# Kernel optimization log

Measured on AMD Instinct MI355X. Metric: run time of the kernel, lower is better.

Reference implementation:

```python
import jax, jax.numpy as jnp
import numpy as np

N = 169343
EPS = 1e-5


def gcn_norm(edge_index, n):
    """GCN normalization with self-loops: returns per-edge norm and per-node self-loop norm."""
    dst = edge_index[1]
    deg = jnp.ones((n,), jnp.float32).at[dst].add(1.0)  # in-degree + self loop
    dinv = jax.lax.rsqrt(deg)
    edge_norm = dinv[edge_index[0]] * dinv[dst]          # [E]
    self_norm = 1.0 / deg                                 # deg^-1/2 * deg^-1/2
    return edge_norm, self_norm


def gcn_conv(x, W, b, edge_index, edge_norm, self_norm):
    h = x @ W                                             # [N, out]
    msg = h[edge_index[0]] * edge_norm[:, None]           # gather + scale, [E, out]
    agg = jax.ops.segment_sum(msg, edge_index[1], num_segments=N)
    return agg + h * self_norm[:, None] + b


def batch_norm(x, gamma, beta, mean, var):
    return (x - mean) * jax.lax.rsqrt(var + EPS) * gamma + beta


def setup_inputs() -> dict:
    key = jax.random.key(0)
    ks = jax.random.split(key, 12)
    E = 2400000
    d_in, d_h, d_out = 128, 256, 40
    inp = {
        "x": jax.random.normal(ks[0], (N, d_in), jnp.float32),
        "edge_index": jax.random.randint(ks[1], (2, E), 0, N, jnp.int64),
        "W1": jax.random.normal(ks[2], (d_in, d_h), jnp.float32) / np.sqrt(d_in),
        "b1": jnp.zeros((d_h,), jnp.float32),
        "g1": 1.0 + 0.1 * jax.random.normal(ks[3], (d_h,), jnp.float32),
        "beta1": 0.1 * jax.random.normal(ks[4], (d_h,), jnp.float32),
        "m1": 0.1 * jax.random.normal(ks[5], (d_h,), jnp.float32),
        "v1": jnp.ones((d_h,), jnp.float32),
        "W2": jax.random.normal(ks[6], (d_h, d_h), jnp.float32) / np.sqrt(d_h),
        "b2": jnp.zeros((d_h,), jnp.float32),
        "g2": 1.0 + 0.1 * jax.random.normal(ks[7], (d_h,), jnp.float32),
        "beta2": 0.1 * jax.random.normal(ks[8], (d_h,), jnp.float32),
        "m2": 0.1 * jax.random.normal(ks[9], (d_h,), jnp.float32),
        "v2": jnp.ones((d_h,), jnp.float32),
        "W3": jax.random.normal(ks[10], (d_h, d_out), jnp.float32) / np.sqrt(d_h),
        "b3": jnp.zeros((d_out,), jnp.float32),
    }
    return inp


def reference(x, edge_index, W1, b1, g1, beta1, m1, v1, W2, b2, g2, beta2, m2, v2, W3, b3):
    # eval mode: BN uses running stats, dropout is identity
    edge_norm, self_norm = gcn_norm(edge_index, N)
    h = gcn_conv(x, W1, b1, edge_index, edge_norm, self_norm)
    h = jax.nn.relu(batch_norm(h, g1, beta1, m1, v1))
    h = gcn_conv(h, W2, b2, edge_index, edge_norm, self_norm)
    h = jax.nn.relu(batch_norm(h, g2, beta2, m2, v2))
    node_embeddings = h
    out = gcn_conv(h, W3, b3, edge_index, edge_norm, self_norm)
    out = jax.nn.log_softmax(out, axis=-1)
    return out, node_embeddings
```

## Files before the change

kernel.cpp:

```cpp
#include <hip/hip_runtime.h>
#include <math.h>

#define EPSV 1e-5f
#define NBMAX 680

typedef __attribute__((ext_vector_type(8))) short bf16x8;
typedef __attribute__((ext_vector_type(4))) float floatx4;

__device__ __forceinline__ unsigned short f32_to_bf16(float f) {
    unsigned int u = __float_as_uint(f);
    unsigned int r = (u + 0x7fffu + ((u >> 16) & 1u)) >> 16;
    return (unsigned short)r;
}
__device__ __forceinline__ float bf16_lo(unsigned int u) { return __uint_as_float(u << 16); }
__device__ __forceinline__ float bf16_hi(unsigned int u) { return __uint_as_float(u & 0xffff0000u); }


__global__ __launch_bounds__(256) void zero_int_kernel(int* __restrict__ p, int n) {
    int i = blockIdx.x * 256 + threadIdx.x;
    if (i < n) p[i] = 0;
}

__global__ __launch_bounds__(256) void bucket_hist_kernel(const int* __restrict__ ei,
                                                          int* __restrict__ hist,
                                                          int* __restrict__ btot,
                                                          int E, int nb) {
    __shared__ int lh[NBMAX];
    int t = threadIdx.x;
    for (int i = t; i < nb; i += 256) lh[i] = 0;
    __syncthreads();
    int chunk = (E + 255) >> 8;
    int beg = blockIdx.x * chunk;
    int end = min(beg + chunk, E);
    for (int e = beg + t; e < end; e += 256) {
        int d = ei[E + e];
        atomicAdd(&lh[d >> 8], 1);
    }
    __syncthreads();
    for (int i = t; i < nb; i += 256) {
        int v = lh[i];
        hist[i * 256 + blockIdx.x] = v;
        if (v) atomicAdd(&btot[i], v);
    }
}

__global__ __launch_bounds__(256) void bucket_offsets_kernel(const int* __restrict__ btot,
                                                             int* __restrict__ hist,
                                                             int* __restrict__ bbase, int E) {
    __shared__ int red[256];
    __shared__ int sa[256], sb[256];
    int b = blockIdx.x, t = threadIdx.x;
    int s = 0;
    for (int i = t; i < b; i += 256) s += btot[i];
    red[t] = s;
    __syncthreads();
    for (int off = 128; off > 0; off >>= 1) {
        if (t < off) red[t] += red[t + off];
        __syncthreads();
    }
    int mybase = red[0];
    if (t == 0) {
        bbase[b] = mybase;
        if (b == gridDim.x - 1) bbase[gridDim.x] = E;
    }
    int orig = hist[b * 256 + t];
    sa[t] = orig;
    __syncthreads();
    int* sp = sa; int* dp = sb;
    for (int off = 1; off < 256; off <<= 1) {
        int x = sp[t] + (t >= off ? sp[t - off] : 0);
        dp[t] = x;
        __syncthreads();
        int* q = sp; sp = dp; dp = q;
    }
    hist[b * 256 + t] = mybase + sp[t] - orig;
}

__global__ __launch_bounds__(256) void bin_kernel(const int* __restrict__ ei,
                                                  const int* __restrict__ hist,
                                                  unsigned int* __restrict__ tmp,
                                                  int E, int nb) {
    __shared__ int cur[NBMAX];
    int t = threadIdx.x;
    for (int i = t; i < nb; i += 256) cur[i] = hist[i * 256 + blockIdx.x];
    __syncthreads();
    int chunk = (E + 255) >> 8;
    int beg = blockIdx.x * chunk;
    int end = min(beg + chunk, E);
    for (int e = beg + t; e < end; e += 256) {
        int s = ei[e];
        int d = ei[E + e];
        int pos = atomicAdd(&cur[d >> 8], 1);
        tmp[pos] = ((unsigned int)(d & 255) << 24) | (unsigned int)s;
    }
}

__global__ __launch_bounds__(256) void bucket_sort_kernel(const unsigned int* __restrict__ tmp,
                                                          const int* __restrict__ bbase,
                                                          int* __restrict__ rowptr,
                                                          int* __restrict__ csr,
                                                          float* __restrict__ dinv,
                                                          float* __restrict__ selfnorm,
                                                          int n, int E) {
    __shared__ int cnt[256];
    __shared__ int sa[256], sb[256];
    int b = blockIdx.x, t = threadIdx.x;
    int node0 = b << 8;
    int nn = min(256, n - node0);
    int ebeg = bbase[b], eend = bbase[b + 1];
    cnt[t] = 0;
    __syncthreads();
    for (int e = ebeg + t; e < eend; e += 256) {
        unsigned int v = tmp[e];
        atomicAdd(&cnt[v >> 24], 1);
    }
    __syncthreads();
    sa[t] = cnt[t];
    __syncthreads();
    int* sp = sa; int* dp = sb;
    for (int off = 1; off < 256; off <<= 1) {
        int x = sp[t] + (t >= off ? sp[t - off] : 0);
        dp[t] = x;
        __syncthreads();
        int* q = sp; sp = dp; dp = q;
    }
    int excl = sp[t] - cnt[t];
    if (t < nn) {
        rowptr[node0 + t] = ebeg + excl;
        float df = (float)(cnt[t] + 1);
        dinv[node0 + t] = rsqrtf(df);
        selfnorm[node0 + t] = 1.0f / df;
    }
    if (b == gridDim.x - 1 && t == 0) rowptr[n] = E;
    dp[t] = ebeg + excl;
    __syncthreads();
    for (int e = ebeg + t; e < eend; e += 256) {
        unsigned int v = tmp[e];
        int lpos = atomicAdd(&dp[v >> 24], 1);
        csr[lpos] = (int)(v & 0xFFFFFFu);
    }
}


__global__ __launch_bounds__(256) void cast_bf16_kernel(const float* __restrict__ in,
                                                        unsigned short* __restrict__ out, int n4) {
    int i = blockIdx.x * 256 + threadIdx.x;
    if (i < n4) {
        float4 f = ((const float4*)in)[i];
        ushort4 o;
        o.x = f32_to_bf16(f.x); o.y = f32_to_bf16(f.y);
        o.z = f32_to_bf16(f.z); o.w = f32_to_bf16(f.w);
        ((ushort4*)out)[i] = o;
    }
}

__global__ __launch_bounds__(256) void cast_transpose_kernel(const float* __restrict__ in,
                                                             unsigned short* __restrict__ out,
                                                             int K, int M) {
    int i = blockIdx.x * 256 + threadIdx.x;
    if (i < K * M) {
        int k = i / M, m2 = i - k * M;
        out[(size_t)m2 * K + k] = f32_to_bf16(in[i]);
    }
}


__device__ __forceinline__ void acc8(float* acc, uint4 u, float wt) {
    acc[0] += wt * bf16_lo(u.x); acc[1] += wt * bf16_hi(u.x);
    acc[2] += wt * bf16_lo(u.y); acc[3] += wt * bf16_hi(u.y);
    acc[4] += wt * bf16_lo(u.z); acc[5] += wt * bf16_hi(u.z);
    acc[6] += wt * bf16_lo(u.w); acc[7] += wt * bf16_hi(u.w);
}

template <int LPN>
__global__ __launch_bounds__(256) void agg_pre_kernel(const unsigned short* __restrict__ h,
                                                      const int* __restrict__ rowptr,
                                                      const int* __restrict__ csr,
                                                      const float* __restrict__ dinv,
                                                      const float* __restrict__ selfnorm,
                                                      unsigned short* __restrict__ z, int n) {
    const int W = LPN * 8;
    int gtid = blockIdx.x * 256 + threadIdx.x;
    int node = gtid / LPN;
    int sub = gtid % LPN;
    if (node >= n) return;
    int fb = sub * 8;
    const unsigned short* hb = h + fb;
    int beg = rowptr[node], end = rowptr[node + 1];

    float acc[8] = {0.f, 0.f, 0.f, 0.f, 0.f, 0.f, 0.f, 0.f};
    int e = beg;
    for (; e + 4 <= end; e += 4) {
        int s0 = csr[e], s1 = csr[e + 1], s2 = csr[e + 2], s3 = csr[e + 3];
        float w0 = dinv[s0], w1 = dinv[s1], w2 = dinv[s2], w3 = dinv[s3];
        uint4 u0 = *(const uint4*)(hb + (size_t)s0 * W);
        uint4 u1 = *(const uint4*)(hb + (size_t)s1 * W);
        uint4 u2 = *(const uint4*)(hb + (size_t)s2 * W);
        uint4 u3 = *(const uint4*)(hb + (size_t)s3 * W);
        acc8(acc, u0, w0); acc8(acc, u1, w1); acc8(acc, u2, w2); acc8(acc, u3, w3);
    }
    for (; e < end; ++e) {
        int s = csr[e];
        float w = dinv[s];
        uint4 u = *(const uint4*)(hb + (size_t)s * W);
        acc8(acc, u, w);
    }
    float di = dinv[node], sn = selfnorm[node];
    uint4 us = *(const uint4*)(hb + (size_t)node * W);
    float hs[8];
    hs[0] = bf16_lo(us.x); hs[1] = bf16_hi(us.x);
    hs[2] = bf16_lo(us.y); hs[3] = bf16_hi(us.y);
    hs[4] = bf16_lo(us.z); hs[5] = bf16_hi(us.z);
    hs[6] = bf16_lo(us.w); hs[7] = bf16_hi(us.w);
    float o[8];
#pragma unroll
    for (int j = 0; j < 8; ++j) o[j] = acc[j] * di + hs[j] * sn;
    uint4 ov;
    ov.x = ((unsigned int)f32_to_bf16(o[1]) << 16) | f32_to_bf16(o[0]);
    ov.y = ((unsigned int)f32_to_bf16(o[3]) << 16) | f32_to_bf16(o[2]);
    ov.z = ((unsigned int)f32_to_bf16(o[5]) << 16) | f32_to_bf16(o[4]);
    ov.w = ((unsigned int)f32_to_bf16(o[7]) << 16) | f32_to_bf16(o[6]);
    *(uint4*)(z + (size_t)node * W + fb) = ov;
}


__global__ __launch_bounds__(256) void gemm_bf16_kernel(
    const unsigned short* __restrict__ A, const unsigned short* __restrict__ Wt,
    unsigned short* __restrict__ Cb, int cstride, float* __restrict__ Cf,
    const float* __restrict__ bias, const float* __restrict__ g,
    const float* __restrict__ beta, const float* __restrict__ m,
    const float* __restrict__ v, int nrows, int K, int M) {
    __shared__ short As[64 * 40];
    __shared__ short Bs[64 * 40];
    int tid = threadIdx.x;
    int wave = tid >> 6, lane = tid & 63;
    int quad = lane >> 4, l16 = lane & 15;
    int wr = (wave >> 1) * 32, wc = (wave & 1) * 32;
    int row0 = blockIdx.x * 64, col0 = blockIdx.y * 64;

    int srow = tid >> 2, sseg = tid & 3;

    floatx4 acc[2][2];
#pragma unroll
    for (int i = 0; i < 2; ++i)
#pragma unroll
        for (int j = 0; j < 2; ++j)
#pragma unroll
            for (int r = 0; r < 4; ++r) acc[i][j][r] = 0.f;

    for (int k0 = 0; k0 < K; k0 += 32) {
        uint4 av = make_uint4(0, 0, 0, 0);
        int gr = row0 + srow;
        if (gr < nrows) av = *(const uint4*)(A + (size_t)gr * K + k0 + sseg * 8);
        uint4 bv = make_uint4(0, 0, 0, 0);
        int gc = col0 + srow;
        if (gc < M) bv = *(const uint4*)(Wt + (size_t)gc * K + k0 + sseg * 8);

        *(uint4*)(As + srow * 40 + sseg * 8) = av;
        *(uint4*)(Bs + srow * 40 + sseg * 8) = bv;
        __syncthreads();

        bf16x8 af[2], bfr[2];
#pragma unroll
        for (int i = 0; i < 2; ++i)
            af[i] = *(const bf16x8*)(As + (wr + i * 16 + l16) * 40 + quad * 8);
#pragma unroll
        for (int j = 0; j < 2; ++j)
            bfr[j] = *(const bf16x8*)(Bs + (wc + j * 16 + l16) * 40 + quad * 8);

#pragma unroll
        for (int i = 0; i < 2; ++i)
#pragma unroll
            for (int j = 0; j < 2; ++j)
                acc[i][j] = __builtin_amdgcn_mfma_f32_16x16x32_bf16(af[i], bfr[j], acc[i][j], 0, 0, 0);
        __syncthreads();
    }

    float sc[2], sh[2];
#pragma unroll
    for (int j = 0; j < 2; ++j) {
        int col = col0 + wc + j * 16 + l16;
        if (bias && col < M) {
            float s = g[col] * rsqrtf(v[col] + EPSV);
            sc[j] = s;
            sh[j] = (bias[col] - m[col]) * s + beta[col];
        } else {
            sc[j] = 1.f; sh[j] = 0.f;
        }
    }

#pragma unroll
    for (int i = 0; i < 2; ++i) {
#pragma unroll
        for (int r = 0; r < 4; ++r) {
            int row = row0 + wr + i * 16 + quad * 4 + r;
            if (row >= nrows) continue;
#pragma unroll
            for (int j = 0; j < 2; ++j) {
                int col = col0 + wc + j * 16 + l16;
                if (col < M) {
                    float val = acc[i][j][r];
                    if (bias) val = fmaxf(val * sc[j] + sh[j], 0.f);
                    if (Cb) Cb[(size_t)row * cstride + col] = f32_to_bf16(val);
                    if (Cf) Cf[(size_t)row * M + col] = val;
                }
            }
        }
    }
}


__global__ __launch_bounds__(256) void agg3_lsm_kernel(const unsigned short* __restrict__ h3,
                                                       const int* __restrict__ rowptr,
                                                       const int* __restrict__ csr,
                                                       const float* __restrict__ dinv,
                                                       const float* __restrict__ selfnorm,
                                                       const float* __restrict__ b3,
                                                       float* __restrict__ out, int n) {
    int node = (blockIdx.x * 256 + threadIdx.x) >> 6;
    int lane = threadIdx.x & 63;
    if (node >= n) return;
    int sub = lane & 15, grp = lane >> 4;
    int beg = rowptr[node], end = rowptr[node + 1];
    const unsigned short* hb = h3 + sub * 4;

    float acc[4] = {0.f, 0.f, 0.f, 0.f};
    int e = beg + grp;
    for (; e + 4 < end; e += 8) {
        int s0 = csr[e], s1 = csr[e + 4];
        float w0 = dinv[s0], w1 = dinv[s1];
        uint2 u0 = *(const uint2*)(hb + (size_t)s0 * 64);
        uint2 u1 = *(const uint2*)(hb + (size_t)s1 * 64);
        acc[0] += w0 * bf16_lo(u0.x); acc[1] += w0 * bf16_hi(u0.x);
        acc[2] += w0 * bf16_lo(u0.y); acc[3] += w0 * bf16_hi(u0.y);
        acc[0] += w1 * bf16_lo(u1.x); acc[1] += w1 * bf16_hi(u1.x);
        acc[2] += w1 * bf16_lo(u1.y); acc[3] += w1 * bf16_hi(u1.y);
    }
    for (; e < end; e += 4) {
        int s = csr[e];
        float w = dinv[s];
        uint2 u = *(const uint2*)(hb + (size_t)s * 64);
        acc[0] += w * bf16_lo(u.x); acc[1] += w * bf16_hi(u.x);
        acc[2] += w * bf16_lo(u.y); acc[3] += w * bf16_hi(u.y);
    }
#pragma unroll
    for (int j = 0; j < 4; ++j) {
        acc[j] += __shfl_xor(acc[j], 16, 64);
        acc[j] += __shfl_xor(acc[j], 32, 64);
    }
    float di = dinv[node], sn = selfnorm[node];
    uint2 us = *(const uint2*)(h3 + (size_t)node * 64 + sub * 4);
    float self4[4] = {bf16_lo(us.x), bf16_hi(us.x), bf16_lo(us.y), bf16_hi(us.y)};
    int f0 = sub * 4;
    float z[4];
#pragma unroll
    for (int j = 0; j < 4; ++j) {
        int f = f0 + j;
        int fc = f < 40 ? f : 0;
        float val = acc[j] * di + self4[j] * sn + b3[fc];
        z[j] = (f < 40) ? val : -INFINITY;
    }
    float mx = fmaxf(fmaxf(z[0], z[1]), fmaxf(z[2], z[3]));
#pragma unroll
    for (int off = 1; off < 16; off <<= 1) mx = fmaxf(mx, __shfl_xor(mx, off, 64));
    float se = expf(z[0] - mx) + expf(z[1] - mx) + expf(z[2] - mx) + expf(z[3] - mx);
#pragma unroll
    for (int off = 1; off < 16; off <<= 1) se += __shfl_xor(se, off, 64);
    float lse = logf(se);
    if (grp == 0 && sub < 10) {
        float4 o = make_float4(z[0] - mx - lse, z[1] - mx - lse, z[2] - mx - lse, z[3] - mx - lse);
        *(float4*)(out + (size_t)node * 40 + f0) = o;
    }
}


extern "C" void kernel_launch(void* const* d_in, const int* in_sizes, int n_in,
                              void* d_out, int out_size, void* d_ws, size_t ws_size,
                              hipStream_t stream) {
    const float* x  = (const float*)d_in[0];
    const int* ei   = (const int*)d_in[1];
    const float* W1 = (const float*)d_in[2];
    const float* b1 = (const float*)d_in[3];
    const float* g1 = (const float*)d_in[4];
    const float* be1 = (const float*)d_in[5];
    const float* m1 = (const float*)d_in[6];
    const float* v1 = (const float*)d_in[7];
    const float* W2 = (const float*)d_in[8];
    const float* b2 = (const float*)d_in[9];
    const float* g2 = (const float*)d_in[10];
    const float* be2 = (const float*)d_in[11];
    const float* m2 = (const float*)d_in[12];
    const float* v2 = (const float*)d_in[13];
    const float* W3 = (const float*)d_in[14];
    const float* b3 = (const float*)d_in[15];

    const int N = in_sizes[0] / 128;
    const int E = in_sizes[1] / 2;
    const int nb = (N + 255) >> 8;

    float* out_lsm = (float*)d_out;
    float* out_emb = (float*)d_out + (size_t)N * 40;

    char* ws = (char*)d_ws;
    size_t off = 0;
    auto carve = [&](size_t bytes) -> void* {
        void* p = ws + off;
        off = (off + bytes + 255) & ~(size_t)255;
        return p;
    };
    int* hist     = (int*)carve((size_t)nb * 256 * 4);
    int* btot     = (int*)carve((size_t)nb * 4);
    int* bbase    = (int*)carve((size_t)(nb + 1) * 4);
    int* rowptr   = (int*)carve((size_t)(N + 1) * 4);
    int* csr      = (int*)carve((size_t)E * 4);
    float* dinv     = (float*)carve((size_t)N * 4);
    float* selfnorm = (float*)carve((size_t)N * 4);
    unsigned short* W1t = (unsigned short*)carve((size_t)256 * 128 * 2);
    unsigned short* W2t = (unsigned short*)carve((size_t)256 * 256 * 2);
    unsigned short* W3t = (unsigned short*)carve((size_t)40 * 256 * 2);
    unsigned short* P1 = (unsigned short*)carve((size_t)N * 256 * 2);
    unsigned short* P2 = (unsigned short*)carve((size_t)N * 256 * 2);
    (void)ws_size; (void)n_in; (void)out_size;

    unsigned short* xbf = P1;
    unsigned short* z1  = P2;
    unsigned short* y1  = P1;
    unsigned short* z2  = P2;
    unsigned short* y2  = P1;
    unsigned short* h3  = P2;
    unsigned int* tmp = (unsigned int*)P2;

    dim3 blk(256);

    hipLaunchKernelGGL(zero_int_kernel, dim3((nb + 255) / 256), blk, 0, stream, btot, nb);
    hipLaunchKernelGGL(bucket_hist_kernel, dim3(256), blk, 0, stream, ei, hist, btot, E, nb);
    hipLaunchKernelGGL(bucket_offsets_kernel, dim3(nb), blk, 0, stream, btot, hist, bbase, E);
    hipLaunchKernelGGL(bin_kernel, dim3(256), blk, 0, stream, ei, hist, tmp, E, nb);
    hipLaunchKernelGGL(bucket_sort_kernel, dim3(nb), blk, 0, stream, tmp, bbase, rowptr, csr,
                       dinv, selfnorm, N, E);

    int xn4 = N * 128 / 4;
    hipLaunchKernelGGL(cast_bf16_kernel, dim3((xn4 + 255) / 256), blk, 0, stream, x, xbf, xn4);
    hipLaunchKernelGGL(cast_transpose_kernel, dim3((128 * 256 + 255) / 256), blk, 0, stream,
                       W1, W1t, 128, 256);
    hipLaunchKernelGGL(cast_transpose_kernel, dim3((256 * 256 + 255) / 256), blk, 0, stream,
                       W2, W2t, 256, 256);
    hipLaunchKernelGGL(cast_transpose_kernel, dim3((256 * 40 + 255) / 256), blk, 0, stream,
                       W3, W3t, 256, 40);

    dim3 ggrid((N + 63) / 64, 4);
    dim3 ggrid3((N + 63) / 64, 1);

    hipLaunchKernelGGL(HIP_KERNEL_NAME(agg_pre_kernel<16>), dim3((N * 16 + 255) / 256), blk, 0,
                       stream, xbf, rowptr, csr, dinv, selfnorm, z1, N);
    hipLaunchKernelGGL(gemm_bf16_kernel, ggrid, blk, 0, stream, z1, W1t, y1, 256,
                       (float*)nullptr, b1, g1, be1, m1, v1, N, 128, 256);
    hipLaunchKernelGGL(HIP_KERNEL_NAME(agg_pre_kernel<32>), dim3((N * 32 + 255) / 256), blk, 0,
                       stream, y1, rowptr, csr, dinv, selfnorm, z2, N);
    hipLaunchKernelGGL(gemm_bf16_kernel, ggrid, blk, 0, stream, z2, W2t, y2, 256,
                       out_emb, b2, g2, be2, m2, v2, N, 256, 256);
    hipLaunchKernelGGL(gemm_bf16_kernel, ggrid3, blk, 0, stream, y2, W3t, h3, 64,
                       (float*)nullptr, (const float*)nullptr, (const float*)nullptr,
                       (const float*)nullptr, (const float*)nullptr, (const float*)nullptr,
                       N, 256, 40);
    hipLaunchKernelGGL(agg3_lsm_kernel, dim3((N + 3) / 4), blk, 0, stream, h3, rowptr, csr,
                       dinv, selfnorm, b3, out_lsm, N);
}
```

Baseline: 967.4 us.

## Keep full A row-block in LDS and loop over column tiles; deepen gather unroll

The GEMM kernel now loads the whole 64-row A block (up to K=256) into shared memory once and loops over all output column tiles inside one block. Previously a grid dimension over columns made each block re-read A from global memory. The B tile is now prefetched into registers one k-step ahead. The aggregation gather loop gains an 8-way unrolled body that issues all feature loads before the weight loads, to expose more memory-level parallelism. The trade-off is higher LDS use (about 33KB per block), which may lower occupancy, and four times fewer blocks with more serial work in each.

```diff
diff --git a/kernel.cpp b/kernel.cpp
--- a/kernel.cpp
+++ b/kernel.cpp
@@ -190,13 +190,26 @@
 
     float acc[8] = {0.f, 0.f, 0.f, 0.f, 0.f, 0.f, 0.f, 0.f};
     int e = beg;
+    for (; e + 8 <= end; e += 8) {
+        int s[8];
+#pragma unroll
+        for (int q = 0; q < 8; ++q) s[q] = csr[e + q];
+        uint4 u[8];
+#pragma unroll
+        for (int q = 0; q < 8; ++q) u[q] = *(const uint4*)(hb + (size_t)s[q] * W);
+        float w[8];
+#pragma unroll
+        for (int q = 0; q < 8; ++q) w[q] = dinv[s[q]];
+#pragma unroll
+        for (int q = 0; q < 8; ++q) acc8(acc, u[q], w[q]);
+    }
     for (; e + 4 <= end; e += 4) {
         int s0 = csr[e], s1 = csr[e + 1], s2 = csr[e + 2], s3 = csr[e + 3];
-        float w0 = dinv[s0], w1 = dinv[s1], w2 = dinv[s2], w3 = dinv[s3];
         uint4 u0 = *(const uint4*)(hb + (size_t)s0 * W);
         uint4 u1 = *(const uint4*)(hb + (size_t)s1 * W);
         uint4 u2 = *(const uint4*)(hb + (size_t)s2 * W);
         uint4 u3 = *(const uint4*)(hb + (size_t)s3 * W);
+        float w0 = dinv[s0], w1 = dinv[s1], w2 = dinv[s2], w3 = dinv[s3];
         acc8(acc, u0, w0); acc8(acc, u1, w1); acc8(acc, u2, w2); acc8(acc, u3, w3);
     }
     for (; e < end; ++e) {
@@ -230,79 +243,94 @@
     const float* __restrict__ bias, const float* __restrict__ g,
     const float* __restrict__ beta, const float* __restrict__ m,
     const float* __restrict__ v, int nrows, int K, int M) {
-    __shared__ short As[64 * 40];
+    __shared__ short As[64 * 264];
     __shared__ short Bs[64 * 40];
     int tid = threadIdx.x;
     int wave = tid >> 6, lane = tid & 63;
     int quad = lane >> 4, l16 = lane & 15;
     int wr = (wave >> 1) * 32, wc = (wave & 1) * 32;
-    int row0 = blockIdx.x * 64, col0 = blockIdx.y * 64;
+    int row0 = blockIdx.x * 64;
+    int lda = K + 8;
 
     int srow = tid >> 2, sseg = tid & 3;
 
-    floatx4 acc[2][2];
-#pragma unroll
-    for (int i = 0; i < 2; ++i)
-#pragma unroll
-        for (int j = 0; j < 2; ++j)
-#pragma unroll
-            for (int r = 0; r < 4; ++r) acc[i][j][r] = 0.f;
-
-    for (int k0 = 0; k0 < K; k0 += 32) {
-        uint4 av = make_uint4(0, 0, 0, 0);
+    {
         int gr = row0 + srow;
-        if (gr < nrows) av = *(const uint4*)(A + (size_t)gr * K + k0 + sseg * 8);
+        for (int k0 = 0; k0 < K; k0 += 32) {
+            uint4 av = make_uint4(0, 0, 0, 0);
+            if (gr < nrows) av = *(const uint4*)(A + (size_t)gr * K + k0 + sseg * 8);
+            *(uint4*)(As + srow * lda + k0 + sseg * 8) = av;
+        }
+    }
+
+    int MT = (M + 63) >> 6;
+    for (int jt = 0; jt < MT; ++jt) {
+        int col0 = jt * 64;
+        floatx4 acc[2][2];
+#pragma unroll
+        for (int i = 0; i < 2; ++i)
+#pragma unroll
+            for (int j = 0; j < 2; ++j)
+#pragma unroll
+                for (int r = 0; r < 4; ++r) acc[i][j][r] = 0.f;
+
+        int gc = col0 + srow;
         uint4 bv = make_uint4(0, 0, 0, 0);
-        int gc = col0 + srow;
-        if (gc < M) bv = *(const uint4*)(Wt + (size_t)gc * K + k0 + sseg * 8);
-
-        *(uint4*)(As + srow * 40 + sseg * 8) = av;
-        *(uint4*)(Bs + srow * 40 + sseg * 8) = bv;
-        __syncthreads();
-
-        bf16x8 af[2], bfr[2];
-#pragma unroll
-        for (int i = 0; i < 2; ++i)
-            af[i] = *(const bf16x8*)(As + (wr + i * 16 + l16) * 40 + quad * 8);
-#pragma unroll
-        for (int j = 0; j < 2; ++j)
-            bfr[j] = *(const bf16x8*)(Bs + (wc + j * 16 + l16) * 40 + quad * 8);
-
-#pragma unroll
-        for (int i = 0; i < 2; ++i)
+        if (gc < M) bv = *(const uint4*)(Wt + (size_t)gc * K + sseg * 8);
+
+        for (int k0 = 0; k0 < K; k0 += 32) {
+            *(uint4*)(Bs + srow * 40 + sseg * 8) = bv;
+            __syncthreads();
+
+            if (k0 + 32 < K) {
+                bv = make_uint4(0, 0, 0, 0);
+                if (gc < M) bv = *(const uint4*)(Wt + (size_t)gc * K + k0 + 32 + sseg * 8);
+            }
+
+            bf16x8 af[2], bfr[2];
+#pragma unroll
+            for (int i = 0; i < 2; ++i)
+                af[i] = *(const bf16x8*)(As + (wr + i * 16 + l16) * lda + k0 + quad * 8);
 #pragma unroll
             for (int j = 0; j < 2; ++j)
-                acc[i][j] = __builtin_amdgcn_mfma_f32_16x16x32_bf16(af[i], bfr[j], acc[i][j], 0, 0, 0);
-        __syncthreads();
-    }
-
-    float sc[2], sh[2];
-#pragma unroll
-    for (int j = 0; j < 2; ++j) {
-        int col = col0 + wc + j * 16 + l16;
-        if (bias && col < M) {
-            float s = g[col] * rsqrtf(v[col] + EPSV);
-            sc[j] = s;
-            sh[j] = (bias[col] - m[col]) * s + beta[col];
-        } else {
-            sc[j] = 1.f; sh[j] = 0.f;
+                bfr[j] = *(const bf16x8*)(Bs + (wc + j * 16 + l16) * 40 + quad * 8);
+
+#pragma unroll
+            for (int i = 0; i < 2; ++i)
+#pragma unroll
+                for (int j = 0; j < 2; ++j)
+                    acc[i][j] = __builtin_amdgcn_mfma_f32_16x16x32_bf16(af[i], bfr[j], acc[i][j], 0, 0, 0);
+            __syncthreads();
         }
-    }
-
-#pragma unroll
-    for (int i = 0; i < 2; ++i) {
-#pragma unroll
-        for (int r = 0; r < 4; ++r) {
-            int row = row0 + wr + i * 16 + quad * 4 + r;
-            if (row >= nrows) continue;
-#pragma unroll
-            for (int j = 0; j < 2; ++j) {
-                int col = col0 + wc + j * 16 + l16;
-                if (col < M) {
-                    float val = acc[i][j][r];
-                    if (bias) val = fmaxf(val * sc[j] + sh[j], 0.f);
-                    if (Cb) Cb[(size_t)row * cstride + col] = f32_to_bf16(val);
-                    if (Cf) Cf[(size_t)row * M + col] = val;
+
+        float sc[2], sh[2];
+#pragma unroll
+        for (int j = 0; j < 2; ++j) {
+            int col = col0 + wc + j * 16 + l16;
+            if (bias && col < M) {
+                float s = g[col] * rsqrtf(v[col] + EPSV);
+                sc[j] = s;
+                sh[j] = (bias[col] - m[col]) * s + beta[col];
+            } else {
+                sc[j] = 1.f; sh[j] = 0.f;
+            }
+        }
+
+#pragma unroll
+        for (int i = 0; i < 2; ++i) {
+#pragma unroll
+            for (int r = 0; r < 4; ++r) {
+                int row = row0 + wr + i * 16 + quad * 4 + r;
+                if (row >= nrows) continue;
+#pragma unroll
+                for (int j = 0; j < 2; ++j) {
+                    int col = col0 + wc + j * 16 + l16;
+                    if (col < M) {
+                        float val = acc[i][j][r];
+                        if (bias) val = fmaxf(val * sc[j] + sh[j], 0.f);
+                        if (Cb) Cb[(size_t)row * cstride + col] = f32_to_bf16(val);
+                        if (Cf) Cf[(size_t)row * M + col] = val;
+                    }
                 }
             }
         }
@@ -448,8 +476,7 @@
     hipLaunchKernelGGL(cast_transpose_kernel, dim3((256 * 40 + 255) / 256), blk, 0, stream,
                        W3, W3t, 256, 40);
 
-    dim3 ggrid((N + 63) / 64, 4);
-    dim3 ggrid3((N + 63) / 64, 1);
+    dim3 ggrid((N + 63) / 64);
 
     hipLaunchKernelGGL(HIP_KERNEL_NAME(agg_pre_kernel<16>), dim3((N * 16 + 255) / 256), blk, 0,
                        stream, xbf, rowptr, csr, dinv, selfnorm, z1, N);
@@ -459,7 +486,7 @@
                        stream, y1, rowptr, csr, dinv, selfnorm, z2, N);
     hipLaunchKernelGGL(gemm_bf16_kernel, ggrid, blk, 0, stream, z2, W2t, y2, 256,
                        out_emb, b2, g2, be2, m2, v2, N, 256, 256);
-    hipLaunchKernelGGL(gemm_bf16_kernel, ggrid3, blk, 0, stream, y2, W3t, h3, 64,
+    hipLaunchKernelGGL(gemm_bf16_kernel, ggrid, blk, 0, stream, y2, W3t, h3, 64,
                        (float*)nullptr, (const float*)nullptr, (const float*)nullptr,
                        (const float*)nullptr, (const float*)nullptr, (const float*)nullptr,
                        N, 256, 40);
```

Result: faster. 948.2 us (-2.0%).
